# Kernel tuning notes

Measured on AMD Instinct MI355X. Metric: run time of the kernel, lower is better.

The kernel has to match this reference:

```python
import jax, jax.numpy as jnp
import numpy as np

N_NODES = 100000
N_EDGES = 1600000
IN_FEATS = 128
HID = 128
OUT_FEATS = 64


def setup_inputs() -> dict:
    key = jax.random.key(0)
    ks = jax.random.split(key, 8)
    node_ids = jnp.arange(N_NODES, dtype=jnp.int64)
    src = jax.random.randint(ks[0], (N_EDGES,), 0, N_NODES, dtype=jnp.int64)
    dst = jax.random.randint(ks[1], (N_EDGES,), 0, N_NODES, dtype=jnp.int64)
    emb = jax.random.normal(ks[2], (N_NODES, IN_FEATS), dtype=jnp.float32)
    W1 = jax.random.normal(ks[3], (IN_FEATS, HID), dtype=jnp.float32) / np.sqrt(IN_FEATS)
    b1 = jnp.zeros((HID,), dtype=jnp.float32)
    W2 = jax.random.normal(ks[4], (HID, OUT_FEATS), dtype=jnp.float32) / np.sqrt(HID)
    b2 = jnp.zeros((OUT_FEATS,), dtype=jnp.float32)
    return {"node_ids": node_ids, "src": src, "dst": dst, "emb": emb,
            "W1": W1, "b1": b1, "W2": W2, "b2": b2}


def _sym_norms(src, dst):
    # DGL GraphConv norm='both': D_out^{-1/2} on source side, D_in^{-1/2} on dest side,
    # degrees clamped to >= 1.
    ones = jnp.ones(src.shape[0], dtype=jnp.float32)
    deg_out = jax.ops.segment_sum(ones, src, num_segments=N_NODES)
    deg_in = jax.ops.segment_sum(ones, dst, num_segments=N_NODES)
    norm_src = jnp.clip(deg_out, 1.0, None) ** -0.5  # [N]
    norm_dst = jnp.clip(deg_in, 1.0, None) ** -0.5   # [N]
    return norm_src, norm_dst


def _spmm(src, dst, h):
    # rst[dst] += h[src]  (sparse adjacency aggregation)
    return jax.ops.segment_sum(h[src], dst, num_segments=N_NODES)


def reference(node_ids, src, dst, emb, W1, b1, W2, b2):
    norm_src, norm_dst = _sym_norms(src, dst)
    h = emb[node_ids]                                   # [N, IN]
    # Layer 1 (IN -> HID, relu): weight applied after aggregation (in <= out)
    h = _spmm(src, dst, h * norm_src[:, None]) * norm_dst[:, None]
    h = jax.nn.relu(h @ W1 + b1)                        # [N, HID]
    # Dropout(0.5) is identity in eval mode.
    # Layer 2 (HID -> OUT): DGL applies weight BEFORE aggregation when in > out
    h = (h @ W2) * norm_src[:, None]                    # [N, OUT]
    h = _spmm(src, dst, h) * norm_dst[:, None] + b2
    return h
```

## Files before the change

### kernel.cpp

```cpp
#include <hip/hip_runtime.h>

#define N_N 100000
#define N_E 1600000
#define SLOTS 48
#define N_PAD 100096

#define BK_SHIFT 9
#define BK_SIZE 512
#define NBKT 196
#define MAXB 10240
#define EPB2 4096
#define NBLK2 ((N_E + EPB2 - 1) / EPB2)
#define EPT 16

#define BINC_BLKS (2 * NBKT)
#define EMB_BLKS 3125
#define W_BLKS 48

typedef unsigned short ushort_t;
typedef unsigned int uint_t;
typedef _Float16 f16x8 __attribute__((ext_vector_type(8)));
typedef float f32x4 __attribute__((ext_vector_type(4)));

__device__ __forceinline__ ushort_t f2h(float f) {
    union { _Float16 h; ushort_t u; } c; c.h = (_Float16)f; return c.u;
}

__device__ __forceinline__ void acc2h(uint_t v, float wv, float& a, float& b) {
    union { uint_t u; _Float16 h[2]; } c; c.u = v;
    a = fmaf((float)c.h[0], wv, a);
    b = fmaf((float)c.h[1], wv, b);
}

__device__ __forceinline__ void addh(uint_t v, float& a, float& b) {
    union { uint_t u; _Float16 h[2]; } c; c.u = v;
    a += (float)c.h[0];
    b += (float)c.h[1];
}

__device__ __forceinline__ uint_t packh2(float a, float b) {
    union { _Float16 h[2]; uint_t u; } p;
    p.h[0] = (_Float16)a; p.h[1] = (_Float16)b;
    return p.u;
}

__global__ void __launch_bounds__(256) k_scatter(
        const int* __restrict__ src, const int* __restrict__ dst,
        int* __restrict__ cur_d, int* __restrict__ cnt_s,
        uint_t* __restrict__ pe_dst) {
    __shared__ int hd[NBKT], od[NBKT];
    int t = threadIdx.x, blk = blockIdx.x;
    for (int i = t; i < NBKT; i += 256) hd[i] = 0;
    __syncthreads();
    int e0 = blk * EPB2;
    int myS[EPT], myD[EPT], myR[EPT];
#pragma unroll
    for (int i = 0; i < EPT; i++) {
        int e = e0 + t + i * 256;
        if (e < N_E) {
            int s = src[e], d = dst[e];
            myS[i] = s; myD[i] = d;
            myR[i] = atomicAdd(&hd[d >> BK_SHIFT], 1);
            atomicAdd(&cnt_s[s], 1);
        }
    }
    __syncthreads();
    for (int i = t; i < NBKT; i += 256) {
        int c = hd[i]; od[i] = c ? atomicAdd(&cur_d[i], c) : 0;
    }
    __syncthreads();
#pragma unroll
    for (int i = 0; i < EPT; i++) {
        int e = e0 + t + i * 256;
        if (e < N_E) {
            int s = myS[i], d = myD[i];
            int rd = od[d >> BK_SHIFT] + myR[i];
            if (rd < MAXB) pe_dst[(size_t)(d >> BK_SHIFT) * MAXB + rd] =
                               (uint_t)s | ((uint_t)(d & 511) << 17);
        }
    }
}

__global__ void __launch_bounds__(512) k_binC_prep(
        const uint_t* __restrict__ pe_dst, const int* __restrict__ cur_d,
        const int* __restrict__ cnt_s,
        int* __restrict__ slots, int* __restrict__ cnt,
        float* __restrict__ nd, float* __restrict__ ns,
        const float* __restrict__ emb, ushort_t* __restrict__ embf,
        const float* __restrict__ W1, const float* __restrict__ W2,
        ushort_t* __restrict__ w1f, ushort_t* __restrict__ w2f) {
    int t = threadIdx.x, bb = blockIdx.x;
    if (bb >= BINC_BLKS) {
        int pb = bb - BINC_BLKS;
        if (pb < EMB_BLKS) {
            int i = pb * 1024 + t;
            const float4* E4 = (const float4*)emb;
            ushort4* O4 = (ushort4*)embf;
            float4 v0 = E4[i], v1 = E4[i + 512];
            ushort4 o0, o1;
            o0.x = f2h(v0.x); o0.y = f2h(v0.y); o0.z = f2h(v0.z); o0.w = f2h(v0.w);
            o1.x = f2h(v1.x); o1.y = f2h(v1.y); o1.z = f2h(v1.z); o1.w = f2h(v1.w);
            O4[i] = o0; O4[i + 512] = o1;
        } else {
            int idx = (pb - EMB_BLKS) * 512 + t;
            int j = idx & 7, l = (idx >> 3) & 63;
            int k = (l >> 4) * 8 + j;
            int n = l & 15;
            if (idx < 16384) {
                int kc = (idx >> 9) & 3, nt = idx >> 11;
                w1f[idx] = f2h(W1[(kc * 32 + k) * 128 + nt * 16 + n]);
            } else {
                int i2 = idx - 16384;
                int kc = (i2 >> 9) & 3, nt = i2 >> 11;
                w2f[i2] = f2h(W2[(kc * 32 + k) * 64 + nt * 16 + n]);
            }
        }
        return;
    }
    if (bb >= NBKT) {
        int n = ((bb - NBKT) << BK_SHIFT) + t;
        if (n < N_N) ns[n] = 1.0f / sqrtf((float)max(cnt_s[n], 1));
        return;
    }
    __shared__ int lc[BK_SIZE];
    for (int i = t; i < BK_SIZE; i += 512) lc[i] = 0;
    __syncthreads();
    int b = bb;
    int cb = min(cur_d[b], MAXB);
    int nbase = b << BK_SHIFT;
    const uint_t* pe = pe_dst + (size_t)b * MAXB;
    for (int e = t; e < cb; e += 512) {
        uint_t ed = pe[e];
        int dloc = (int)(ed >> 17);
        int s = (int)(ed & 0x1ffffu);
        int pos = atomicAdd(&lc[dloc], 1);
        if (pos < SLOTS) slots[(size_t)(nbase + dloc) * SLOTS + pos] = s;
    }
    __syncthreads();
    for (int i = t; i < BK_SIZE; i += 512) {
        int n = nbase + i;
        if (n < N_N) {
            int c = lc[i];
            cnt[n] = c;
            nd[n] = 1.0f / sqrtf((float)max(c, 1));
        }
    }
}

__global__ void __launch_bounds__(256) k_spmm1(
        const int* __restrict__ cnt, const int* __restrict__ slots,
        const ushort_t* __restrict__ embf, const float* __restrict__ ns,
        const float* __restrict__ nd, uint_t* __restrict__ aggf) {
    int wid = (blockIdx.x * 256 + (int)threadIdx.x) >> 6;
    int node = __builtin_amdgcn_readfirstlane(wid);
    if (node >= N_N) return;
    int lane = threadIdx.x & 63;
    int h = lane >> 5, w32 = lane & 31;
    const int* row = slots + node * SLOTS;
    int len = min(cnt[node], SLOTS);
    const uint2* E2 = (const uint2*)embf;
    float a0 = 0.f, a1 = 0.f, a2 = 0.f, a3 = 0.f;
    int e = 0;
    int n16 = len & ~15;
    for (; e < n16; e += 16) {
        const int* rp = row + e + h;
        int s0 = rp[0],  s1 = rp[2],  s2 = rp[4],  s3 = rp[6];
        int s4 = rp[8],  s5 = rp[10], s6 = rp[12], s7 = rp[14];
        float w0 = ns[s0], w1 = ns[s1], w2 = ns[s2], w3 = ns[s3];
        float w4 = ns[s4], w5 = ns[s5], w6 = ns[s6], w7 = ns[s7];
        uint2 v0 = E2[(size_t)s0 * 32 + w32];
        uint2 v1 = E2[(size_t)s1 * 32 + w32];
        uint2 v2 = E2[(size_t)s2 * 32 + w32];
        uint2 v3 = E2[(size_t)s3 * 32 + w32];
        uint2 v4 = E2[(size_t)s4 * 32 + w32];
        uint2 v5 = E2[(size_t)s5 * 32 + w32];
        uint2 v6 = E2[(size_t)s6 * 32 + w32];
        uint2 v7 = E2[(size_t)s7 * 32 + w32];
        acc2h(v0.x, w0, a0, a1); acc2h(v0.y, w0, a2, a3);
        acc2h(v1.x, w1, a0, a1); acc2h(v1.y, w1, a2, a3);
        acc2h(v2.x, w2, a0, a1); acc2h(v2.y, w2, a2, a3);
        acc2h(v3.x, w3, a0, a1); acc2h(v3.y, w3, a2, a3);
        acc2h(v4.x, w4, a0, a1); acc2h(v4.y, w4, a2, a3);
        acc2h(v5.x, w5, a0, a1); acc2h(v5.y, w5, a2, a3);
        acc2h(v6.x, w6, a0, a1); acc2h(v6.y, w6, a2, a3);
        acc2h(v7.x, w7, a0, a1); acc2h(v7.y, w7, a2, a3);
    }
    int n4 = len & ~3;
    for (; e < n4; e += 4) {
        const int* rp = row + e + h;
        int s0 = rp[0], s1 = rp[2];
        float w0 = ns[s0], w1 = ns[s1];
        uint2 v0 = E2[(size_t)s0 * 32 + w32];
        uint2 v1 = E2[(size_t)s1 * 32 + w32];
        acc2h(v0.x, w0, a0, a1); acc2h(v0.y, w0, a2, a3);
        acc2h(v1.x, w1, a0, a1); acc2h(v1.y, w1, a2, a3);
    }
    for (; e + 1 < len; e += 2) {
        int s = row[e + h];
        float w = ns[s];
        uint2 v = E2[(size_t)s * 32 + w32];
        acc2h(v.x, w, a0, a1); acc2h(v.y, w, a2, a3);
    }
    if (e < len && h == 0) {
        int s = row[e];
        float w = ns[s];
        uint2 v = E2[(size_t)s * 32 + w32];
        acc2h(v.x, w, a0, a1); acc2h(v.y, w, a2, a3);
    }
    a0 += __shfl_xor(a0, 32);
    a1 += __shfl_xor(a1, 32);
    a2 += __shfl_xor(a2, 32);
    a3 += __shfl_xor(a3, 32);
    if (h == 0) {
        float sc = nd[node];
        uint2 o;
        o.x = packh2(a0 * sc, a1 * sc);
        o.y = packh2(a2 * sc, a3 * sc);
        ((uint2*)(aggf + (size_t)node * 64))[w32] = o;
    }
}

#define HSTH 136
__global__ void __launch_bounds__(256, 2) k_gemm(
        const ushort_t* __restrict__ aggf, const ushort_t* __restrict__ w1f,
        const float* __restrict__ b1, const ushort_t* __restrict__ w2f,
        const float* __restrict__ ns, ushort_t* __restrict__ h2b) {
    __shared__ ushort_t sh[128 * HSTH];
    int t = threadIdx.x;
    int w = t >> 6, l = t & 63;
    int quad = l >> 4, lm = l & 15;
    int nb0 = blockIdx.x * 128;

    f16x8 a[2][4];
#pragma unroll
    for (int rt = 0; rt < 2; rt++)
#pragma unroll
        for (int kc = 0; kc < 4; kc++)
            a[rt][kc] = *(const f16x8*)(aggf
                + (size_t)(nb0 + rt * 64 + w * 16 + lm) * 128 + kc * 32 + quad * 8);

    f32x4 acc[2][8];
#pragma unroll
    for (int rt = 0; rt < 2; rt++)
#pragma unroll
        for (int nt = 0; nt < 8; nt++) acc[rt][nt] = (f32x4){0.f, 0.f, 0.f, 0.f};

#pragma unroll
    for (int kc = 0; kc < 4; kc++) {
        f16x8 bq[8];
#pragma unroll
        for (int nt = 0; nt < 8; nt++)
            bq[nt] = *(const f16x8*)(w1f + (((nt * 4 + kc) * 64 + l) << 3));
#pragma unroll
        for (int nt = 0; nt < 8; nt++) {
            acc[0][nt] = __builtin_amdgcn_mfma_f32_16x16x32_f16(a[0][kc], bq[nt], acc[0][nt], 0, 0, 0);
            acc[1][nt] = __builtin_amdgcn_mfma_f32_16x16x32_f16(a[1][kc], bq[nt], acc[1][nt], 0, 0, 0);
        }
    }
#pragma unroll
    for (int nt = 0; nt < 8; nt++) {
        float bb = b1[nt * 16 + lm];
#pragma unroll
        for (int rt = 0; rt < 2; rt++)
#pragma unroll
            for (int r = 0; r < 4; r++) {
                int row = rt * 64 + w * 16 + quad * 4 + r;
                sh[row * HSTH + nt * 16 + lm] = f2h(fmaxf(acc[rt][nt][r] + bb, 0.f));
            }
    }
    __syncthreads();

    f16x8 hh[2][4];
#pragma unroll
    for (int rt = 0; rt < 2; rt++)
#pragma unroll
        for (int kc = 0; kc < 4; kc++)
            hh[rt][kc] = *(const f16x8*)(sh + (rt * 64 + w * 16 + lm) * HSTH
                                         + kc * 32 + quad * 8);

    f32x4 acc2[2][4];
#pragma unroll
    for (int rt = 0; rt < 2; rt++)
#pragma unroll
        for (int q = 0; q < 4; q++) acc2[rt][q] = (f32x4){0.f, 0.f, 0.f, 0.f};

#pragma unroll
    for (int kc = 0; kc < 4; kc++) {
        f16x8 b2q[4];
#pragma unroll
        for (int q = 0; q < 4; q++)
            b2q[q] = *(const f16x8*)(w2f + (((q * 4 + kc) * 64 + l) << 3));
#pragma unroll
        for (int q = 0; q < 4; q++) {
            acc2[0][q] = __builtin_amdgcn_mfma_f32_16x16x32_f16(hh[0][kc], b2q[q], acc2[0][q], 0, 0, 0);
            acc2[1][q] = __builtin_amdgcn_mfma_f32_16x16x32_f16(hh[1][kc], b2q[q], acc2[1][q], 0, 0, 0);
        }
    }
#pragma unroll
    for (int rt = 0; rt < 2; rt++)
#pragma unroll
        for (int r = 0; r < 4; r++) {
            int node = nb0 + rt * 64 + w * 16 + quad * 4 + r;
            if (node < N_N) {
                float s = ns[node];
#pragma unroll
                for (int q = 0; q < 4; q++)
                    h2b[(size_t)node * 64 + q * 16 + lm] = f2h(acc2[rt][q][r] * s);
            }
        }
}

__global__ void __launch_bounds__(256) k_spmm2(
        const int* __restrict__ cnt, const int* __restrict__ slots,
        const ushort_t* __restrict__ h2b, const float* __restrict__ nd,
        const float* __restrict__ b2, float* __restrict__ out) {
    int wid = (blockIdx.x * 256 + (int)threadIdx.x) >> 6;
    int node = __builtin_amdgcn_readfirstlane(wid);
    if (node >= N_N) return;
    int lane = threadIdx.x & 63;
    int q = lane >> 4, w16 = lane & 15;
    const int* row = slots + node * SLOTS;
    int len = min(cnt[node], SLOTS);
    const uint2* H2 = (const uint2*)h2b;
    float a0 = 0.f, a1 = 0.f, a2 = 0.f, a3 = 0.f;
    int e = 0;
    int n16 = len & ~15;
    for (; e < n16; e += 16) {
        const int* rp = row + e + q;
        int s0 = rp[0], s1 = rp[4], s2 = rp[8], s3 = rp[12];
        uint2 v0 = H2[(size_t)s0 * 16 + w16];
        uint2 v1 = H2[(size_t)s1 * 16 + w16];
        uint2 v2 = H2[(size_t)s2 * 16 + w16];
        uint2 v3 = H2[(size_t)s3 * 16 + w16];
        addh(v0.x, a0, a1); addh(v0.y, a2, a3);
        addh(v1.x, a0, a1); addh(v1.y, a2, a3);
        addh(v2.x, a0, a1); addh(v2.y, a2, a3);
        addh(v3.x, a0, a1); addh(v3.y, a2, a3);
    }
    int n4 = len & ~3;
    for (; e < n4; e += 4) {
        int s = row[e + q];
        uint2 v = H2[(size_t)s * 16 + w16];
        addh(v.x, a0, a1); addh(v.y, a2, a3);
    }
    if (e < len && q < len - e) {
        int s = row[e + q];
        uint2 v = H2[(size_t)s * 16 + w16];
        addh(v.x, a0, a1); addh(v.y, a2, a3);
    }
    a0 += __shfl_xor(a0, 16); a1 += __shfl_xor(a1, 16);
    a2 += __shfl_xor(a2, 16); a3 += __shfl_xor(a3, 16);
    a0 += __shfl_xor(a0, 32); a1 += __shfl_xor(a1, 32);
    a2 += __shfl_xor(a2, 32); a3 += __shfl_xor(a3, 32);
    if (q == 0) {
        float sc = nd[node];
        float4 bb = ((const float4*)b2)[w16];
        float4 o;
        o.x = a0 * sc + bb.x;
        o.y = a1 * sc + bb.y;
        o.z = a2 * sc + bb.z;
        o.w = a3 * sc + bb.w;
        ((float4*)(out + (size_t)node * 64))[w16] = o;
    }
}

extern "C" void kernel_launch(void* const* d_in, const int* in_sizes, int n_in,
                              void* d_out, int out_size, void* d_ws, size_t ws_size,
                              hipStream_t stream) {
    const int* src = (const int*)d_in[1];
    const int* dst = (const int*)d_in[2];
    const float* emb = (const float*)d_in[3];
    const float* W1 = (const float*)d_in[4];
    const float* b1 = (const float*)d_in[5];
    const float* W2 = (const float*)d_in[6];
    const float* b2 = (const float*)d_in[7];
    float* out = (float*)d_out;

    int* cur_d   = (int*)d_ws;
    int* cnt_s   = cur_d + 256;
    int* cnt     = cnt_s + N_PAD;
    float* ns    = (float*)(cnt + N_PAD);
    float* nd    = ns + N_PAD;
    int* slots   = (int*)(nd + N_PAD);
    uint_t* pe_dst = (uint_t*)(slots + (size_t)N_N * SLOTS);
    ushort_t* embf = (ushort_t*)(pe_dst + (size_t)NBKT * MAXB);
    uint_t* aggf = (uint_t*)(embf + (size_t)N_PAD * 128);
    ushort_t* w1f = (ushort_t*)(aggf + (size_t)N_PAD * 64);
    ushort_t* w2f = w1f + 16384;
    ushort_t* h2b = w2f + 8192;

    hipMemsetAsync(cur_d, 0, sizeof(int) * (256 + N_PAD), stream);
    k_scatter  <<<NBLK2, 256, 0, stream>>>(src, dst, cur_d, cnt_s, pe_dst);
    k_binC_prep<<<BINC_BLKS + EMB_BLKS + W_BLKS, 512, 0, stream>>>(
        pe_dst, cur_d, cnt_s, slots, cnt, nd, ns, emb, embf, W1, W2, w1f, w2f);
    k_spmm1 <<<(N_N + 3) / 4, 256, 0, stream>>>(cnt, slots, embf, ns, nd, aggf);
    k_gemm  <<<N_PAD / 128, 256, 0, stream>>>((const ushort_t*)aggf, w1f, b1, w2f, ns, h2b);
    k_spmm2 <<<(N_N + 3) / 4, 256, 0, stream>>>(cnt, slots, h2b, nd, b2, out);
}
```

Baseline: 337.0 us.

## Bucket source edges in LDS instead of global atomics for out-degree counting

Random global atomicAdds on cnt_s for the source-degree count are replaced with a second LDS bucket histogram per block. Source ids are written into per-bucket pe_src arrays, and binC_prep counts them in shared memory to produce ns. Edges per block are halved, which gives more blocks and fewer registers per thread. The cost is extra global writes and reads of a 1.6M-entry array, plus a smaller memset.

```diff
diff --git a/kernel.cpp b/kernel.cpp
--- a/kernel.cpp
+++ b/kernel.cpp
@@ -9,9 +9,9 @@
 #define BK_SIZE 512
 #define NBKT 196
 #define MAXB 10240
-#define EPB2 4096
+#define EPB2 2048
 #define NBLK2 ((N_E + EPB2 - 1) / EPB2)
-#define EPT 16
+#define EPT 8
 
 #define BINC_BLKS (2 * NBKT)
 #define EMB_BLKS 3125
@@ -46,27 +46,30 @@
 
 __global__ void __launch_bounds__(256) k_scatter(
         const int* __restrict__ src, const int* __restrict__ dst,
-        int* __restrict__ cur_d, int* __restrict__ cnt_s,
-        uint_t* __restrict__ pe_dst) {
-    __shared__ int hd[NBKT], od[NBKT];
+        int* __restrict__ cur_d, int* __restrict__ cur_s,
+        uint_t* __restrict__ pe_dst, uint_t* __restrict__ pe_src) {
+    __shared__ int hd[NBKT], hs[NBKT], od[NBKT], os_[NBKT];
     int t = threadIdx.x, blk = blockIdx.x;
-    for (int i = t; i < NBKT; i += 256) hd[i] = 0;
+    for (int i = t; i < NBKT; i += 256) { hd[i] = 0; hs[i] = 0; }
     __syncthreads();
     int e0 = blk * EPB2;
-    int myS[EPT], myD[EPT], myR[EPT];
+    int myS[EPT], myD[EPT];
+    uint_t myR[EPT];
 #pragma unroll
     for (int i = 0; i < EPT; i++) {
         int e = e0 + t + i * 256;
         if (e < N_E) {
             int s = src[e], d = dst[e];
             myS[i] = s; myD[i] = d;
-            myR[i] = atomicAdd(&hd[d >> BK_SHIFT], 1);
-            atomicAdd(&cnt_s[s], 1);
+            uint_t rd = (uint_t)atomicAdd(&hd[d >> BK_SHIFT], 1);
+            uint_t rs = (uint_t)atomicAdd(&hs[s >> BK_SHIFT], 1);
+            myR[i] = rd | (rs << 16);
         }
     }
     __syncthreads();
     for (int i = t; i < NBKT; i += 256) {
-        int c = hd[i]; od[i] = c ? atomicAdd(&cur_d[i], c) : 0;
+        int c = hd[i]; od[i]  = c ? atomicAdd(&cur_d[i], c) : 0;
+        c = hs[i];     os_[i] = c ? atomicAdd(&cur_s[i], c) : 0;
     }
     __syncthreads();
 #pragma unroll
@@ -74,16 +77,18 @@
         int e = e0 + t + i * 256;
         if (e < N_E) {
             int s = myS[i], d = myD[i];
-            int rd = od[d >> BK_SHIFT] + myR[i];
+            int rd = od[d >> BK_SHIFT] + (int)(myR[i] & 0xffffu);
+            int rs = os_[s >> BK_SHIFT] + (int)(myR[i] >> 16);
             if (rd < MAXB) pe_dst[(size_t)(d >> BK_SHIFT) * MAXB + rd] =
                                (uint_t)s | ((uint_t)(d & 511) << 17);
+            if (rs < MAXB) pe_src[(size_t)(s >> BK_SHIFT) * MAXB + rs] = (uint_t)s;
         }
     }
 }
 
 __global__ void __launch_bounds__(512) k_binC_prep(
-        const uint_t* __restrict__ pe_dst, const int* __restrict__ cur_d,
-        const int* __restrict__ cnt_s,
+        const uint_t* __restrict__ pe_dst, const uint_t* __restrict__ pe_src,
+        const int* __restrict__ cur_d, const int* __restrict__ cur_s,
         int* __restrict__ slots, int* __restrict__ cnt,
         float* __restrict__ nd, float* __restrict__ ns,
         const float* __restrict__ emb, ushort_t* __restrict__ embf,
@@ -117,32 +122,41 @@
         }
         return;
     }
-    if (bb >= NBKT) {
-        int n = ((bb - NBKT) << BK_SHIFT) + t;
-        if (n < N_N) ns[n] = 1.0f / sqrtf((float)max(cnt_s[n], 1));
-        return;
-    }
     __shared__ int lc[BK_SIZE];
     for (int i = t; i < BK_SIZE; i += 512) lc[i] = 0;
     __syncthreads();
-    int b = bb;
-    int cb = min(cur_d[b], MAXB);
-    int nbase = b << BK_SHIFT;
-    const uint_t* pe = pe_dst + (size_t)b * MAXB;
-    for (int e = t; e < cb; e += 512) {
-        uint_t ed = pe[e];
-        int dloc = (int)(ed >> 17);
-        int s = (int)(ed & 0x1ffffu);
-        int pos = atomicAdd(&lc[dloc], 1);
-        if (pos < SLOTS) slots[(size_t)(nbase + dloc) * SLOTS + pos] = s;
-    }
-    __syncthreads();
-    for (int i = t; i < BK_SIZE; i += 512) {
-        int n = nbase + i;
-        if (n < N_N) {
-            int c = lc[i];
-            cnt[n] = c;
-            nd[n] = 1.0f / sqrtf((float)max(c, 1));
+    if (bb < NBKT) {
+        int b = bb;
+        int cb = min(cur_d[b], MAXB);
+        int nbase = b << BK_SHIFT;
+        const uint_t* pe = pe_dst + (size_t)b * MAXB;
+        for (int e = t; e < cb; e += 512) {
+            uint_t ed = pe[e];
+            int dloc = (int)(ed >> 17);
+            int s = (int)(ed & 0x1ffffu);
+            int pos = atomicAdd(&lc[dloc], 1);
+            if (pos < SLOTS) slots[(size_t)(nbase + dloc) * SLOTS + pos] = s;
+        }
+        __syncthreads();
+        for (int i = t; i < BK_SIZE; i += 512) {
+            int n = nbase + i;
+            if (n < N_N) {
+                int c = lc[i];
+                cnt[n] = c;
+                nd[n] = 1.0f / sqrtf((float)max(c, 1));
+            }
+        }
+    } else {
+        int b = bb - NBKT;
+        int cb = min(cur_s[b], MAXB);
+        int nbase = b << BK_SHIFT;
+        const uint_t* pe = pe_src + (size_t)b * MAXB;
+        for (int e = t; e < cb; e += 512)
+            atomicAdd(&lc[(int)pe[e] - nbase], 1);
+        __syncthreads();
+        for (int i = t; i < BK_SIZE; i += 512) {
+            int n = nbase + i;
+            if (n < N_N) ns[n] = 1.0f / sqrtf((float)max(lc[i], 1));
         }
     }
 }
@@ -377,22 +391,23 @@
     float* out = (float*)d_out;
 
     int* cur_d   = (int*)d_ws;
-    int* cnt_s   = cur_d + 256;
-    int* cnt     = cnt_s + N_PAD;
+    int* cur_s   = cur_d + 256;
+    int* cnt     = cur_s + 256;
     float* ns    = (float*)(cnt + N_PAD);
     float* nd    = ns + N_PAD;
     int* slots   = (int*)(nd + N_PAD);
     uint_t* pe_dst = (uint_t*)(slots + (size_t)N_N * SLOTS);
-    ushort_t* embf = (ushort_t*)(pe_dst + (size_t)NBKT * MAXB);
+    uint_t* pe_src = pe_dst + (size_t)NBKT * MAXB;
+    ushort_t* embf = (ushort_t*)(pe_src + (size_t)NBKT * MAXB);
     uint_t* aggf = (uint_t*)(embf + (size_t)N_PAD * 128);
     ushort_t* w1f = (ushort_t*)(aggf + (size_t)N_PAD * 64);
     ushort_t* w2f = w1f + 16384;
     ushort_t* h2b = w2f + 8192;
 
-    hipMemsetAsync(cur_d, 0, sizeof(int) * (256 + N_PAD), stream);
-    k_scatter  <<<NBLK2, 256, 0, stream>>>(src, dst, cur_d, cnt_s, pe_dst);
+    hipMemsetAsync(cur_d, 0, sizeof(int) * 512, stream);
+    k_scatter  <<<NBLK2, 256, 0, stream>>>(src, dst, cur_d, cur_s, pe_dst, pe_src);
     k_binC_prep<<<BINC_BLKS + EMB_BLKS + W_BLKS, 512, 0, stream>>>(
-        pe_dst, cur_d, cnt_s, slots, cnt, nd, ns, emb, embf, W1, W2, w1f, w2f);
+        pe_dst, pe_src, cur_d, cur_s, slots, cnt, nd, ns, emb, embf, W1, W2, w1f, w2f);
     k_spmm1 <<<(N_N + 3) / 4, 256, 0, stream>>>(cnt, slots, embf, ns, nd, aggf);
     k_gemm  <<<N_PAD / 128, 256, 0, stream>>>((const ushort_t*)aggf, w1f, b1, w2f, ns, h2b);
     k_spmm2 <<<(N_N + 3) / 4, 256, 0, stream>>>(cnt, slots, h2b, nd, b2, out);
```

Measured after the change: 299.6 us. 11.1% less time.
